# Kernel optimization log

Hardware: AMD Instinct MI355X
Metric: run time of the kernel (lower is better)

## Reference

```python
import jax, jax.numpy as jnp
import numpy as np

WINDOWS = ((0, 4), (2, 6), (4, 8))
N_CLASSES = 64
EPS = 1e-12  # F.normalize eps


def setup_inputs() -> dict:
    key = jax.random.key(0)
    k1, k2 = jax.random.split(key)
    S, Q, T, D = 256, 4096, 8, 1024
    support_features = jax.random.normal(k1, (S, T, D), dtype=jnp.float32)
    target_features = jax.random.normal(k2, (Q, T, D), dtype=jnp.float32)
    support_labels = jnp.arange(S, dtype=jnp.int32) % N_CLASSES  # 4 shots per class, sorted-unique order
    logit_scale = jnp.array(0.0, dtype=jnp.float32)
    fusion_logits = jnp.zeros((3,), dtype=jnp.float32)
    return {
        'support_features': support_features,
        'target_features': target_features,
        'support_labels': support_labels,
        'logit_scale': logit_scale,
        'fusion_logits': fusion_logits,
    }


def _l2norm(x):
    n = jnp.sqrt(jnp.sum(x * x, axis=-1, keepdims=True))
    return x / jnp.maximum(n, EPS)


def _pairwise_dist(query_seq, support_seq):
    # query_seq: [Q, Tq, D], support_seq: [K, Ts, D] -> 1 - cosine sim [Q, K, Tq, Ts]
    sim = jnp.einsum('qtd,ksd->qkts', _l2norm(query_seq), _l2norm(support_seq))
    return 1.0 - sim


def _bi_mhm(dists):
    # dists: [Q, K, Tq, Ts]
    return dists.min(axis=3).sum(axis=2) + dists.min(axis=2).sum(axis=2)


def _segments(features):
    # features: [N, T, D] -> [N, n_windows, D] (mean over each window)
    return jnp.stack([features[:, s:e, :].mean(axis=1) for s, e in WINDOWS], axis=1)


def _prototypes(features, labels):
    # scatter-mean over class labels; features: [S, ...], labels: [S]
    sums = jax.ops.segment_sum(features, labels, num_segments=N_CLASSES)
    counts = jax.ops.segment_sum(jnp.ones((features.shape[0],), features.dtype), labels,
                                 num_segments=N_CLASSES)
    return sums / counts[:, None, None]


def reference(support_features, target_features, support_labels, logit_scale, fusion_logits):
    # global (frame-level) bidirectional min-sum chamfer distance to class prototypes
    support_proto = _prototypes(support_features, support_labels)          # [K, T, D]
    global_dist = _bi_mhm(_pairwise_dist(target_features, support_proto))  # [Q, K]

    # segment-level distances
    support_segments = _segments(support_features)                          # [S, 3, D]
    target_segments = _segments(target_features)                            # [Q, 3, D]
    support_seg_proto = _prototypes(support_segments, support_labels)       # [K, 3, D]
    seg_dist = _pairwise_dist(target_segments, support_seg_proto)           # [Q, K, 3, 3]
    seg_q2s = seg_dist.min(axis=3).sum(axis=2)
    seg_s2q = seg_dist.min(axis=2).sum(axis=2)

    fusion = jax.nn.softmax(fusion_logits)
    fused = (fusion[0] * global_dist + fusion[1] * seg_s2q + fusion[2] * seg_q2s)
    fused = fused * jnp.exp(logit_scale)
    return (-fused, -global_dist, -seg_s2q, -seg_q2s)
```

## Files before the change

### kernel.cpp

```cpp
#include <hip/hip_runtime.h>
#include <stdint.h>

typedef unsigned short u16;
typedef short short8 __attribute__((ext_vector_type(8)));
typedef float floatx4 __attribute__((ext_vector_type(4)));

#define KDIM 1024
#define QN   4096
#define KCLS 64
#define QK   (QN * KCLS)
#define NKT  16

#define DPP_XOR1 0xB1
#define DPP_XOR2 0x4E
#define DPP_HMIR 0x141
#define SWZ_XOR6  0x181F
#define SWZ_XOR16 0x401F

template <int CTRL>
__device__ __forceinline__ float dppf(float x) {
  int r = __builtin_amdgcn_mov_dpp(__builtin_bit_cast(int, x), CTRL, 0xF, 0xF, true);
  return __builtin_bit_cast(float, r);
}
template <int OFF>
__device__ __forceinline__ float swzf(float x) {
  int r = __builtin_amdgcn_ds_swizzle(__builtin_bit_cast(int, x), OFF);
  return __builtin_bit_cast(float, r);
}
__device__ __forceinline__ float max8(float x) {
  x = fmaxf(x, dppf<DPP_XOR1>(x));
  x = fmaxf(x, dppf<DPP_XOR2>(x));
  x = fmaxf(x, dppf<DPP_HMIR>(x));
  return x;
}
__device__ __forceinline__ float sum8(float x) {
  x += dppf<DPP_XOR1>(x);
  x += dppf<DPP_XOR2>(x);
  x += dppf<DPP_HMIR>(x);
  return x;
}


__device__ __forceinline__ u16 f2bf(float x) {
  union { float f; uint32_t u; } un; un.f = x;
  uint32_t u = un.u;
  u += 0x7FFFu + ((u >> 16) & 1u);
  return (u16)(u >> 16);
}

struct alignas(16) F4 { float x, y, z, w; };
struct alignas(8)  U16x4 { u16 a, b, c, d; };

__device__ __forceinline__ float dot4(const F4& a, const F4& b) {
  return a.x*b.x + a.y*b.y + a.z*b.z + a.w*b.w;
}

__device__ __forceinline__ float inv_norm(float ss) {
  return 1.0f / fmaxf(sqrtf(ss), 1e-12f);
}

#define SB()    __builtin_amdgcn_s_barrier()
#define SCHED() __builtin_amdgcn_sched_barrier(0)

__device__ __forceinline__ void load_lds16(const u16* g, u16* l) {
  __builtin_amdgcn_global_load_lds((__attribute__((address_space(1))) void*)(g),
                                   (__attribute__((address_space(3))) void*)(l),
                                   16, 0, 0);
}

__global__ __launch_bounds__(256) void prep_B(const float* __restrict__ S,
                                              u16* __restrict__ Bg,
                                              float* __restrict__ invnS,
                                              float* __restrict__ invnSw) {
  __shared__ float sb[4][12];
  const int k = blockIdx.x, tid = threadIdx.x;
  const int lane = tid & 63, wave = tid >> 6;

  F4 p[8];
  #pragma unroll
  for (int t = 0; t < 8; ++t) { p[t].x = 0.f; p[t].y = 0.f; p[t].z = 0.f; p[t].w = 0.f; }
  #pragma unroll
  for (int s = 0; s < 4; ++s)
    #pragma unroll
    for (int t = 0; t < 8; ++t) {
      const F4 v = *(const F4*)(S + (size_t)(((s*64 + k)*8 + t))*1024 + tid*4);
      p[t].x += v.x; p[t].y += v.y; p[t].z += v.z; p[t].w += v.w;
    }
  float ss[11], tot[11];
  #pragma unroll
  for (int t = 0; t < 8; ++t) ss[t] = dot4(p[t], p[t]) * 0.0625f;
  #pragma unroll
  for (int w = 0; w < 3; ++w) {
    F4 y;
    y.x = (p[2*w].x + p[2*w+1].x + p[2*w+2].x + p[2*w+3].x) * 0.0625f;
    y.y = (p[2*w].y + p[2*w+1].y + p[2*w+2].y + p[2*w+3].y) * 0.0625f;
    y.z = (p[2*w].z + p[2*w+1].z + p[2*w+2].z + p[2*w+3].z) * 0.0625f;
    y.w = (p[2*w].w + p[2*w+1].w + p[2*w+2].w + p[2*w+3].w) * 0.0625f;
    ss[8+w] = dot4(y, y);
  }
  #pragma unroll
  for (int v = 0; v < 11; ++v) {
    float x = ss[v];
    #pragma unroll
    for (int m = 1; m < 64; m <<= 1) x += __shfl_xor(x, m);
    ss[v] = x;
  }
  if (lane == 0) {
    #pragma unroll
    for (int v = 0; v < 11; ++v) sb[wave][v] = ss[v];
  }
  __syncthreads();
  #pragma unroll
  for (int v = 0; v < 11; ++v)
    tot[v] = sb[0][v] + sb[1][v] + sb[2][v] + sb[3][v];

  #pragma unroll
  for (int t = 0; t < 8; ++t) {
    U16x4 o; o.a = f2bf(p[t].x*0.25f); o.b = f2bf(p[t].y*0.25f);
    o.c = f2bf(p[t].z*0.25f); o.d = f2bf(p[t].w*0.25f);
    *(U16x4*)(Bg + (size_t)(k*8 + t)*1024 + tid*4) = o;
  }
  if (tid < 8)       invnS [k*8 + tid]     = inv_norm(tot[tid]);
  else if (tid < 11) invnSw[k*4 + tid - 8] = inv_norm(tot[tid]) * 0.0625f;
}

__global__ __launch_bounds__(512, 1) void fused_all(const float* __restrict__ T,
                                                    const u16* __restrict__ Bg,
                                                    const float* __restrict__ invnS,
                                                    const float* __restrict__ invnSw,
                                                    float* __restrict__ outF,
                                                    float* __restrict__ outG,
                                                    float* __restrict__ outS2Q,
                                                    float* __restrict__ outQ2S,
                                                    const float* __restrict__ fl,
                                                    const float* __restrict__ ls) {
  __shared__ __align__(16) u16 At[128 * 64];
  __shared__ __align__(16) u16 Bt[2][512 * 64];

  const int tid  = threadIdx.x;
  const int lane = tid & 63;
  const int wave = tid >> 6;
  const int wm = wave >> 1;
  const int wn = wave & 1;
  const int bx = blockIdx.x;

  const int srow8 = lane >> 3, sl8 = lane & 7;
  const int scolB = (sl8 ^ srow8) * 8;

  const float* Tw = T + ((size_t)bx * 128 + wave * 16) * KDIM + lane;

  floatx4 acc[2][16] = {};
  float ssRow[16] = {};
  float ssW0[3] = {}, ssW1[3] = {};
  float x[16];
  short8 af[2][2];

  const int m16 = lane & 15, g4 = lane >> 4, r7 = lane & 7;

  auto stageB = [&](int t) {
    u16* dst = &Bt[t & 1][0];
    #pragma unroll
    for (int r = 0; r < 8; ++r) {
      const int c = wave * 8 + r;
      const int row = c * 8 + srow8;
      load_lds16(Bg + (size_t)row * KDIM + t * 64 + scolB, dst + c * 512);
    }
  };
  auto loadX = [&](int t) {
    #pragma unroll
    for (int r = 0; r < 16; ++r) x[r] = Tw[(size_t)r * KDIM + t * 64];
  };
  auto cvtWriteNorm = [&]() {
    #pragma unroll
    for (int r = 0; r < 16; ++r) {
      const int row = wave * 16 + r;
      At[row * 64 + (((lane >> 3) ^ (r & 7)) * 8) + (lane & 7)] = f2bf(x[r]);
      ssRow[r] += x[r] * x[r];
    }
    #pragma unroll
    for (int w = 0; w < 3; ++w) {
      const float a0 = (x[2*w] + x[2*w+1] + x[2*w+2] + x[2*w+3]) * 0.25f;
      ssW0[w] += a0 * a0;
      const float a1 = (x[8+2*w] + x[8+2*w+1] + x[8+2*w+2] + x[8+2*w+3]) * 0.25f;
      ssW1[w] += a1 * a1;
    }
  };
  auto ldA = [&]() {
    #pragma unroll
    for (int i = 0; i < 2; ++i)
      #pragma unroll
      for (int s = 0; s < 2; ++s) {
        const int row = wm * 32 + i * 16 + m16;
        af[i][s] = *(const short8*)&At[row * 64 + (((s * 4 + g4) ^ r7) * 8)];
      }
  };
  auto mfmaPhase = [&](int buf) {
    const u16* Bb = &Bt[buf][0];
    #pragma unroll
    for (int jc = 0; jc < 8; ++jc) {
      short8 bf[2][2];
      #pragma unroll
      for (int j2 = 0; j2 < 2; ++j2)
        #pragma unroll
        for (int s = 0; s < 2; ++s) {
          const int rowb = wn * 256 + (jc * 2 + j2) * 16 + m16;
          bf[j2][s] = *(const short8*)&Bb[rowb * 64 + (((s * 4 + g4) ^ r7) * 8)];
        }
      #pragma unroll
      for (int i = 0; i < 2; ++i)
        #pragma unroll
        for (int j2 = 0; j2 < 2; ++j2)
          #pragma unroll
          for (int s = 0; s < 2; ++s)
            acc[i][jc * 2 + j2] = __builtin_amdgcn_mfma_f32_16x16x32_bf16(
                af[i][s], bf[j2][s], acc[i][jc * 2 + j2], 0, 0, 0);
    }
  };

  loadX(0);
  stageB(0);
  cvtWriteNorm();
  SCHED();
  asm volatile("s_waitcnt vmcnt(0) lgkmcnt(0)");
  SCHED();
  SB(); SCHED();

  #pragma unroll 1
  for (int t = 0; t < NKT; ++t) {
    ldA();
    if (t < NKT - 1) { loadX(t + 1); stageB(t + 1); }
    SCHED();
    asm volatile("s_waitcnt lgkmcnt(0)");
    SCHED();
    SB(); SCHED();
    mfmaPhase(t & 1);
    if (t < NKT - 1) cvtWriteNorm();
    SCHED();
    asm volatile("s_waitcnt vmcnt(0) lgkmcnt(0)");
    SCHED();
    SB(); SCHED();
  }

  float* invT_l  = (float*)At;
  float* invTw_l = invT_l + 128;
  #pragma unroll
  for (int r = 0; r < 16; ++r) {
    float v = ssRow[r];
    #pragma unroll
    for (int mk = 1; mk < 64; mk <<= 1) v += __shfl_xor(v, mk);
    if (lane == 0) invT_l[wave * 16 + r] = inv_norm(v);
  }
  #pragma unroll
  for (int w = 0; w < 3; ++w) {
    float v0 = ssW0[w], v1 = ssW1[w];
    #pragma unroll
    for (int mk = 1; mk < 64; mk <<= 1) { v0 += __shfl_xor(v0, mk); v1 += __shfl_xor(v1, mk); }
    if (lane == 0) {
      invTw_l[(wave * 2 + 0) * 3 + w] = inv_norm(v0);
      invTw_l[(wave * 2 + 1) * 3 + w] = inv_norm(v1);
    }
  }
  __syncthreads();

  const int sIdx = lane & 7;
  const int b3 = (lane >> 3) & 1;
  const int b4 = (lane >> 4) & 1;
  const int b5 = lane >> 5;

  float invT[2][4], invTw3[2][3], invS[16], invSw3[16][3];
  #pragma unroll
  for (int i = 0; i < 2; ++i) {
    const int ql = wm * 4 + i * 2 + b5;
    #pragma unroll
    for (int r = 0; r < 4; ++r) invT[i][r] = invT_l[ql * 8 + b4 * 4 + r];
    #pragma unroll
    for (int w = 0; w < 3; ++w) invTw3[i][w] = invTw_l[ql * 3 + w];
  }
  #pragma unroll
  for (int j = 0; j < 16; ++j) {
    const int k = wn * 32 + j * 2 + b3;
    invS[j] = invnS[k * 8 + sIdx];
    #pragma unroll
    for (int v = 0; v < 3; ++v) invSw3[j][v] = invnSw[k * 4 + v];
  }

  const float f0 = fl[0], f1 = fl[1], f2 = fl[2];
  const float mx = fmaxf(f0, fmaxf(f1, f2));
  const float e0 = __expf(f0 - mx), e1 = __expf(f1 - mx), e2 = __expf(f2 - mx);
  const float sc = __expf(ls[0]) / (e0 + e1 + e2);

  const int vA = (sIdx < 4) ? 0 : 2;
  const bool v1ok = (sIdx >= 2) && (sIdx <= 5);

  #pragma unroll
  for (int i = 0; i < 2; ++i) {
    #pragma unroll
    for (int j = 0; j < 16; ++j) {
      const floatx4 c = acc[i][j];

      float sim[4];
      #pragma unroll
      for (int r = 0; r < 4; ++r) sim[r] = c[r] * invT[i][r] * invS[j];
      float rs = 0.f;
      #pragma unroll
      for (int r = 0; r < 4; ++r) rs += max8(sim[r]);
      rs += swzf<SWZ_XOR16>(rs);
      float cm = fmaxf(fmaxf(sim[0], sim[1]), fmaxf(sim[2], sim[3]));
      cm = fmaxf(cm, swzf<SWZ_XOR16>(cm));
      const float cs = sum8(cm);
      const float g = rs + cs - 16.0f;

      float wA[4], wB[4];
      #pragma unroll
      for (int r = 0; r < 4; ++r) {
        const float p2 = c[r] + dppf<DPP_XOR1>(c[r]);
        wA[r] = p2 + dppf<DPP_XOR2>(p2);
        wB[r] = p2 + swzf<SWZ_XOR6>(p2);
      }
      float twA[3], twB[3];
      {
        const float aAll = wA[0] + wA[1] + wA[2] + wA[3];
        const float aOth = swzf<SWZ_XOR16>(aAll);
        twA[0] = b4 ? aOth : aAll;
        twA[2] = b4 ? aAll : aOth;
        const float aH = b4 ? (wA[0] + wA[1]) : (wA[2] + wA[3]);
        twA[1] = aH + swzf<SWZ_XOR16>(aH);
        const float bAll = wB[0] + wB[1] + wB[2] + wB[3];
        const float bOth = swzf<SWZ_XOR16>(bAll);
        twB[0] = b4 ? bOth : bAll;
        twB[2] = b4 ? bAll : bOth;
        const float bH = b4 ? (wB[0] + wB[1]) : (wB[2] + wB[3]);
        twB[1] = bH + swzf<SWZ_XOR16>(bH);
      }
      float pA[3], pB[3];
      #pragma unroll
      for (int w = 0; w < 3; ++w) {
        pA[w] = twA[w] * invTw3[i][w] * invSw3[j][vA];
        pB[w] = twB[w] * invTw3[i][w] * invSw3[j][1];
      }
      float q2s = 0.f;
      #pragma unroll
      for (int w = 0; w < 3; ++w)
        q2s += max8(v1ok ? fmaxf(pA[w], pB[w]) : pA[w]);
      const float mwA = fmaxf(fmaxf(pA[0], pA[1]), pA[2]);
      const float mwB = fmaxf(fmaxf(pB[0], pB[1]), pB[2]);
      float contrib = ((sIdx == 0) | (sIdx == 4)) ? mwA : 0.f;
      if (sIdx == 2) contrib += mwB;
      const float s2q = sum8(contrib);

      if ((lane & 23) == 0) {
        const int q = bx * 16 + wm * 4 + i * 2 + b5;
        const int k = wn * 32 + j * 2 + b3;
        const size_t idx = (size_t)q * KCLS + k;
        const float o1 = g;
        const float o2 = s2q - 3.0f;
        const float o3 = q2s - 3.0f;
        outG[idx]   = o1;
        outS2Q[idx] = o2;
        outQ2S[idx] = o3;
        outF[idx]   = sc * (e0 * o1 + e1 * o2 + e2 * o3);
      }
    }
  }
}


extern "C" void kernel_launch(void* const* d_in, const int* in_sizes, int n_in,
                              void* d_out, int out_size, void* d_ws, size_t ws_size,
                              hipStream_t stream) {
  (void)in_sizes; (void)n_in; (void)out_size; (void)ws_size;
  const float* S  = (const float*)d_in[0];
  const float* T  = (const float*)d_in[1];
  const float* ls = (const float*)d_in[3];
  const float* fl = (const float*)d_in[4];

  float* outF   = (float*)d_out;
  float* outG   = outF + QK;
  float* outS2Q = outF + 2 * (size_t)QK;
  float* outQ2S = outF + 3 * (size_t)QK;

  u16*   Bg     = (u16*)d_ws;
  float* invnS  = (float*)(Bg + (size_t)512 * 1024);
  float* invnSw = invnS + 512;

  prep_B<<<KCLS, 256, 0, stream>>>(S, Bg, invnS, invnSw);

  fused_all<<<256, 512, 0, stream>>>(T, Bg, invnS, invnSw,
                                     outF, outG, outS2Q, outQ2S, fl, ls);
}
```

Measured before the change: 265.3 us.

## Split fused kernel into 2D grid of smaller blocks with double-buffered A tile

Result: slower. 274.9 us (+3.6%).

```diff
diff --git a/kernel.cpp b/kernel.cpp
--- a/kernel.cpp
+++ b/kernel.cpp
@@ -124,7 +124,7 @@
   else if (tid < 11) invnSw[k*4 + tid - 8] = inv_norm(tot[tid]) * 0.0625f;
 }
 
-__global__ __launch_bounds__(512, 1) void fused_all(const float* __restrict__ T,
+__global__ __launch_bounds__(256, 2) void fused_all(const float* __restrict__ T,
                                                     const u16* __restrict__ Bg,
                                                     const float* __restrict__ invnS,
                                                     const float* __restrict__ invnSw,
@@ -134,22 +134,24 @@
                                                     float* __restrict__ outQ2S,
                                                     const float* __restrict__ fl,
                                                     const float* __restrict__ ls) {
-  __shared__ __align__(16) u16 At[128 * 64];
-  __shared__ __align__(16) u16 Bt[2][512 * 64];
+  __shared__ __align__(16) u16 At[2][64 * 64];
+  __shared__ __align__(16) u16 Bt[2][256 * 64];
 
   const int tid  = threadIdx.x;
   const int lane = tid & 63;
   const int wave = tid >> 6;
   const int wm = wave >> 1;
   const int wn = wave & 1;
-  const int bx = blockIdx.x;
+  const int px = blockIdx.x;
+  const int ny = blockIdx.y;
 
   const int srow8 = lane >> 3, sl8 = lane & 7;
   const int scolB = (sl8 ^ srow8) * 8;
-
-  const float* Tw = T + ((size_t)bx * 128 + wave * 16) * KDIM + lane;
-
-  floatx4 acc[2][16] = {};
+  const u16* Bh = Bg + (size_t)ny * 256 * KDIM;
+
+  const float* Tw = T + ((size_t)px * 64 + wave * 16) * KDIM + lane;
+
+  floatx4 acc[2][8] = {};
   float ssRow[16] = {};
   float ssW0[3] = {}, ssW1[3] = {};
   float x[16];
@@ -163,18 +165,18 @@
     for (int r = 0; r < 8; ++r) {
       const int c = wave * 8 + r;
       const int row = c * 8 + srow8;
-      load_lds16(Bg + (size_t)row * KDIM + t * 64 + scolB, dst + c * 512);
+      load_lds16(Bh + (size_t)row * KDIM + t * 64 + scolB, dst + c * 512);
     }
   };
   auto loadX = [&](int t) {
     #pragma unroll
     for (int r = 0; r < 16; ++r) x[r] = Tw[(size_t)r * KDIM + t * 64];
   };
-  auto cvtWriteNorm = [&]() {
+  auto cvtWriteNorm = [&](int buf) {
     #pragma unroll
     for (int r = 0; r < 16; ++r) {
       const int row = wave * 16 + r;
-      At[row * 64 + (((lane >> 3) ^ (r & 7)) * 8) + (lane & 7)] = f2bf(x[r]);
+      At[buf][row * 64 + (((lane >> 3) ^ (r & 7)) * 8) + (lane & 7)] = f2bf(x[r]);
       ssRow[r] += x[r] * x[r];
     }
     #pragma unroll
@@ -185,25 +187,25 @@
       ssW1[w] += a1 * a1;
     }
   };
-  auto ldA = [&]() {
+  auto ldA = [&](int buf) {
     #pragma unroll
     for (int i = 0; i < 2; ++i)
       #pragma unroll
       for (int s = 0; s < 2; ++s) {
         const int row = wm * 32 + i * 16 + m16;
-        af[i][s] = *(const short8*)&At[row * 64 + (((s * 4 + g4) ^ r7) * 8)];
+        af[i][s] = *(const short8*)&At[buf][row * 64 + (((s * 4 + g4) ^ r7) * 8)];
       }
   };
   auto mfmaPhase = [&](int buf) {
     const u16* Bb = &Bt[buf][0];
     #pragma unroll
-    for (int jc = 0; jc < 8; ++jc) {
+    for (int jc = 0; jc < 4; ++jc) {
       short8 bf[2][2];
       #pragma unroll
       for (int j2 = 0; j2 < 2; ++j2)
         #pragma unroll
         for (int s = 0; s < 2; ++s) {
-          const int rowb = wn * 256 + (jc * 2 + j2) * 16 + m16;
+          const int rowb = wn * 128 + (jc * 2 + j2) * 16 + m16;
           bf[j2][s] = *(const short8*)&Bb[rowb * 64 + (((s * 4 + g4) ^ r7) * 8)];
         }
       #pragma unroll
@@ -219,30 +221,28 @@
 
   loadX(0);
   stageB(0);
-  cvtWriteNorm();
+  cvtWriteNorm(0);
   SCHED();
-  asm volatile("s_waitcnt vmcnt(0) lgkmcnt(0)");
+  asm volatile("s_waitcnt vmcnt(0) lgkmcnt(0)" ::: "memory");
   SCHED();
   SB(); SCHED();
 
   #pragma unroll 1
   for (int t = 0; t < NKT; ++t) {
-    ldA();
+    const int buf = t & 1;
+    ldA(buf);
     if (t < NKT - 1) { loadX(t + 1); stageB(t + 1); }
     SCHED();
-    asm volatile("s_waitcnt lgkmcnt(0)");
+    mfmaPhase(buf);
+    if (t < NKT - 1) cvtWriteNorm(buf ^ 1);
+    SCHED();
+    asm volatile("s_waitcnt vmcnt(0) lgkmcnt(0)" ::: "memory");
     SCHED();
     SB(); SCHED();
-    mfmaPhase(t & 1);
-    if (t < NKT - 1) cvtWriteNorm();
-    SCHED();
-    asm volatile("s_waitcnt vmcnt(0) lgkmcnt(0)");
-    SCHED();
-    SB(); SCHED();
   }
 
   float* invT_l  = (float*)At;
-  float* invTw_l = invT_l + 128;
+  float* invTw_l = invT_l + 64;
   #pragma unroll
   for (int r = 0; r < 16; ++r) {
     float v = ssRow[r];
@@ -266,8 +266,9 @@
   const int b3 = (lane >> 3) & 1;
   const int b4 = (lane >> 4) & 1;
   const int b5 = lane >> 5;
-
-  float invT[2][4], invTw3[2][3], invS[16], invSw3[16][3];
+  const int kL = ny * 32 + wn * 16;
+
+  float invT[2][4], invTw3[2][3], invS[8], invSw3[8][3];
   #pragma unroll
   for (int i = 0; i < 2; ++i) {
     const int ql = wm * 4 + i * 2 + b5;
@@ -277,8 +278,8 @@
     for (int w = 0; w < 3; ++w) invTw3[i][w] = invTw_l[ql * 3 + w];
   }
   #pragma unroll
-  for (int j = 0; j < 16; ++j) {
-    const int k = wn * 32 + j * 2 + b3;
+  for (int j = 0; j < 8; ++j) {
+    const int k = kL + j * 2 + b3;
     invS[j] = invnS[k * 8 + sIdx];
     #pragma unroll
     for (int v = 0; v < 3; ++v) invSw3[j][v] = invnSw[k * 4 + v];
@@ -295,7 +296,7 @@
   #pragma unroll
   for (int i = 0; i < 2; ++i) {
     #pragma unroll
-    for (int j = 0; j < 16; ++j) {
+    for (int j = 0; j < 8; ++j) {
       const floatx4 c = acc[i][j];
 
       float sim[4];
@@ -349,8 +350,8 @@
       const float s2q = sum8(contrib);
 
       if ((lane & 23) == 0) {
-        const int q = bx * 16 + wm * 4 + i * 2 + b5;
-        const int k = wn * 32 + j * 2 + b3;
+        const int q = px * 8 + wm * 4 + i * 2 + b5;
+        const int k = kL + j * 2 + b3;
         const size_t idx = (size_t)q * KCLS + k;
         const float o1 = g;
         const float o2 = s2q - 3.0f;
@@ -385,6 +386,6 @@
 
   prep_B<<<KCLS, 256, 0, stream>>>(S, Bg, invnS, invnSw);
 
-  fused_all<<<256, 512, 0, stream>>>(T, Bg, invnS, invnSw,
-                                     outF, outG, outS2Q, outQ2S, fl, ls);
-}
+  fused_all<<<dim3(512, 2), 256, 0, stream>>>(T, Bg, invnS, invnSw,
+                                              outF, outG, outS2Q, outQ2S, fl, ls);
+}
```
